# Kernel optimization log

Hardware: AMD Instinct MI355X
Metric: run time of the kernel (lower is better)

Reference implementation:

```python
import jax, jax.numpy as jnp
import numpy as np

H = 512                      # hidden_dim
C, T, F = 2, 128, 257        # output_dims
FLAT = C * T * F             # 65792 flattened spectrogram frame
CD, SD = 256, 256            # content_dim, style_dim
D_IN = CD + SD + FLAT        # GRU input size


def setup_inputs() -> dict:
    key = jax.random.key(0)
    ks = jax.random.split(key, 8)
    B, S = 4, 16
    sc = 0.02  # small init so tanh/sigmoid stay in a sane range
    return {
        "content_emb": jax.random.normal(ks[0], (B, S, CD), jnp.float32),
        "style_emb": jax.random.normal(ks[1], (B, SD), jnp.float32),
        "start_token": jax.random.normal(ks[2], (FLAT,), jnp.float32),
        "W_ih": jax.random.normal(ks[3], (3 * H, D_IN), jnp.float32) * sc,
        "W_hh": jax.random.normal(ks[4], (3 * H, H), jnp.float32) * sc,
        "b_ih": jnp.zeros((3 * H,), jnp.float32),
        "b_hh": jnp.zeros((3 * H,), jnp.float32),
        "W_proj": jax.random.normal(ks[5], (FLAT, H), jnp.float32) * sc,
        "b_proj": jnp.zeros((FLAT,), jnp.float32),
    }


def _gru_cell(x, h, W_ih, W_hh, b_ih, b_hh):
    # PyTorch GRU gate order: r, z, n
    gi = x @ W_ih.T + b_ih          # (B, 3H)
    gh = h @ W_hh.T + b_hh          # (B, 3H)
    i_r, i_z, i_n = jnp.split(gi, 3, axis=-1)
    h_r, h_z, h_n = jnp.split(gh, 3, axis=-1)
    r = jax.nn.sigmoid(i_r + h_r)
    z = jax.nn.sigmoid(i_z + h_z)
    n = jnp.tanh(i_n + r * h_n)
    return (1.0 - z) * n + z * h


def reference(content_emb, style_emb, start_token, W_ih, W_hh, b_ih, b_hh, W_proj, b_proj):
    B, S, _ = content_emb.shape
    h0 = jnp.zeros((B, H), content_emb.dtype)
    prev0 = jnp.broadcast_to(start_token, (B, FLAT))

    def step(carry, c_s):
        h, prev = carry
        # concat [content_s, style, prev_output] -> (B, D_IN)
        x = jnp.concatenate([c_s, style_emb, prev], axis=-1)
        h = _gru_cell(x, h, W_ih, W_hh, b_ih, b_hh)
        out = h @ W_proj.T + b_proj   # (B, FLAT)
        return (h, out), out

    _, outs = jax.lax.scan(step, (h0, prev0), jnp.swapaxes(content_emb, 0, 1))
    outs = jnp.swapaxes(outs, 0, 1)   # (B, S, FLAT)
    return outs.reshape(B, S, C, T, F)
```

## Files before the change

kernel.cpp:

```cpp
#include <hip/hip_runtime.h>
#include <hip/hip_bf16.h>
#include <math.h>

typedef __bf16 bf16x8 __attribute__((ext_vector_type(8)));
typedef float  f32x4  __attribute__((ext_vector_type(4)));

#define HDIM   512
#define FLAT   65792
#define DIN    66304
#define G3     1536
#define NSLAB  2056
#define NPAD   544
#define LPITCH 40
#define MT     128
#define KSPLIT 21
#define CHUNK  98

#define BH_BYTES  71581696ULL
#define MBUF_BYTES 3342336ULL
#define GIB_BYTES   393216ULL
#define HALL_BYTES  131072ULL
#define HBF_BYTES    65536ULL

__device__ __forceinline__ ushort f2bf(float f) {
    uint u = __float_as_uint(f);
    u += 0x7FFFu + ((u >> 16) & 1u);
    return (ushort)(u >> 16);
}

__global__ __launch_bounds__(256) void buildBh(const float* __restrict__ Wp,
                                               const float* __restrict__ bproj,
                                               const float* __restrict__ start,
                                               ushort* __restrict__ Bh) {
    __shared__ ushort tr[512 * 33];
    const int slab = blockIdx.x;
    const int tid  = threadIdx.x;
    for (int idx = tid; idx < 32 * 512; idx += 256) {
        const int k = idx >> 9;
        const int n = idx & 511;
        tr[n * 33 + k] = f2bf(Wp[(size_t)(slab * 32 + k) * 512 + n]);
    }
    __syncthreads();
    uint* out = (uint*)(Bh + (size_t)slab * 17408);
    for (int d = tid; d < 8704; d += 256) {
        const int n  = d >> 4;
        const int k2 = (d & 15) * 2;
        ushort lo, hi;
        if (n < 512)      { lo = tr[n * 33 + k2];            hi = tr[n * 33 + k2 + 1]; }
        else if (n == 512){ lo = f2bf(bproj[slab * 32 + k2]); hi = f2bf(bproj[slab * 32 + k2 + 1]); }
        else if (n == 513){ lo = f2bf(start[slab * 32 + k2]); hi = f2bf(start[slab * 32 + k2 + 1]); }
        else              { lo = 0; hi = 0; }
        out[d] = (uint)lo | ((uint)hi << 16);
    }
}

__global__ __launch_bounds__(1024) void gemmM(const float* __restrict__ Wih,
                                              const ushort* __restrict__ Bh,
                                              float* __restrict__ Mbuf) {
    __shared__ ushort Alds[MT * LPITCH];
    __shared__ ushort Blds[NPAD * LPITCH];
    const int tid  = threadIdx.x;
    const int lane = tid & 63;
    const int wave = tid >> 6;
    const int wm   = wave >> 1;
    const int wn   = wave & 1;
    const int lrow = lane & 15;
    const int quad = lane >> 4;
    const int bid   = blockIdx.x;
    const int mtile = bid % 12;
    const int kc    = bid / 12;
    const int s0 = kc * CHUNK;
    const int s1 = min(s0 + CHUNK, NSLAB);

    const int arow = tid >> 3;
    const int aseg = tid & 7;
    const float* aPtr = Wih + (size_t)(mtile * MT + arow) * DIN + 512 + aseg * 4;

    f32x4 acc[17];
#pragma unroll
    for (int t = 0; t < 17; ++t) acc[t] = (f32x4){0.f, 0.f, 0.f, 0.f};

    float4 aReg;
    uint4  bReg0 = {}, bReg1 = {}, bReg2 = {};
    {
        const size_t sb = (size_t)s0 * 17408;
        aReg  = *(const float4*)(aPtr + (size_t)s0 * 32);
        bReg0 = *(const uint4*)(Bh + sb + (size_t)tid * 8);
        bReg1 = *(const uint4*)(Bh + sb + (size_t)(tid + 1024) * 8);
        if (tid < 128) bReg2 = *(const uint4*)(Bh + sb + (size_t)(tid + 2048) * 8);
    }
    for (int s = s0; s < s1; ++s) {
        {
            uint2 ap;
            ap.x = (uint)f2bf(aReg.x) | ((uint)f2bf(aReg.y) << 16);
            ap.y = (uint)f2bf(aReg.z) | ((uint)f2bf(aReg.w) << 16);
            *(uint2*)&Alds[arow * LPITCH + aseg * 4] = ap;
            *(uint4*)&Blds[(tid >> 2) * LPITCH + (tid & 3) * 8] = bReg0;
            const int c1 = tid + 1024;
            *(uint4*)&Blds[(c1 >> 2) * LPITCH + (c1 & 3) * 8] = bReg1;
            if (tid < 128) {
                const int c2 = tid + 2048;
                *(uint4*)&Blds[(c2 >> 2) * LPITCH + (c2 & 3) * 8] = bReg2;
            }
        }
        __syncthreads();
        if (s + 1 < s1) {
            const size_t sb = (size_t)(s + 1) * 17408;
            aReg  = *(const float4*)(aPtr + (size_t)(s + 1) * 32);
            bReg0 = *(const uint4*)(Bh + sb + (size_t)tid * 8);
            bReg1 = *(const uint4*)(Bh + sb + (size_t)(tid + 1024) * 8);
            if (tid < 128) bReg2 = *(const uint4*)(Bh + sb + (size_t)(tid + 2048) * 8);
        }
        const bf16x8 af = __builtin_bit_cast(bf16x8,
            *(const uint4*)&Alds[(wm * 16 + lrow) * LPITCH + quad * 8]);
#pragma unroll
        for (int t = 0; t < 17; ++t) {
            const bf16x8 bf = __builtin_bit_cast(bf16x8,
                *(const uint4*)&Blds[(wn * 272 + t * 16 + lrow) * LPITCH + quad * 8]);
            acc[t] = __builtin_amdgcn_mfma_f32_16x16x32_bf16(af, bf, acc[t], 0, 0, 0);
        }
        __syncthreads();
    }
#pragma unroll
    for (int t = 0; t < 17; ++t) {
        const int col = wn * 272 + t * 16 + lrow;
#pragma unroll
        for (int r = 0; r < 4; ++r) {
            const int row = mtile * MT + wm * 16 + quad * 4 + r;
            atomicAdd(&Mbuf[(size_t)row * NPAD + col], acc[t][r]);
        }
    }
}

__global__ __launch_bounds__(1024) void gemmMDirect(const float* __restrict__ Wih,
                                                    const float* __restrict__ Wp,
                                                    const float* __restrict__ bproj,
                                                    const float* __restrict__ start,
                                                    float* __restrict__ Mbuf) {
    __shared__ ushort Alds[MT * LPITCH];
    __shared__ ushort Blds[NPAD * LPITCH];
    const int tid  = threadIdx.x;
    const int lane = tid & 63;
    const int wave = tid >> 6;
    const int wm   = wave >> 1;
    const int wn   = wave & 1;
    const int lrow = lane & 15;
    const int quad = lane >> 4;
    const int bid   = blockIdx.x;
    const int mtile = bid % 12;
    const int kc    = bid / 12;
    const int s0 = kc * CHUNK;
    const int s1 = min(s0 + CHUNK, NSLAB);

    const int arow = tid >> 3;
    const int aseg = tid & 7;
    const float* aPtr = Wih + (size_t)(mtile * MT + arow) * DIN + 512 + aseg * 4;

    const int bk = tid >> 5;
    const int bn0 = (tid & 31) * 4;
    const int ek = tid & 31;
    const float* esrc = (tid < 32) ? bproj : start;

    for (int idx = tid; idx < 30 * LPITCH; idx += 1024) Blds[514 * LPITCH + idx] = 0;

    f32x4 acc[17];
#pragma unroll
    for (int t = 0; t < 17; ++t) acc[t] = (f32x4){0.f, 0.f, 0.f, 0.f};

    float4 aReg;
    float4 bReg[4];
    float  eReg = 0.f;
    {
        aReg = *(const float4*)(aPtr + (size_t)s0 * 32);
        const float* bbase = Wp + (size_t)(s0 * 32 + bk) * 512 + bn0;
#pragma unroll
        for (int q = 0; q < 4; ++q) bReg[q] = *(const float4*)(bbase + q * 128);
        if (tid < 64) eReg = esrc[s0 * 32 + ek];
    }
    for (int s = s0; s < s1; ++s) {
        {
            uint2 ap;
            ap.x = (uint)f2bf(aReg.x) | ((uint)f2bf(aReg.y) << 16);
            ap.y = (uint)f2bf(aReg.z) | ((uint)f2bf(aReg.w) << 16);
            *(uint2*)&Alds[arow * LPITCH + aseg * 4] = ap;
#pragma unroll
            for (int q = 0; q < 4; ++q) {
                const int n = bn0 + q * 128;
                Blds[(n + 0) * LPITCH + bk] = f2bf(bReg[q].x);
                Blds[(n + 1) * LPITCH + bk] = f2bf(bReg[q].y);
                Blds[(n + 2) * LPITCH + bk] = f2bf(bReg[q].z);
                Blds[(n + 3) * LPITCH + bk] = f2bf(bReg[q].w);
            }
            if (tid < 64) Blds[(512 + (tid >> 5)) * LPITCH + ek] = f2bf(eReg);
        }
        __syncthreads();
        if (s + 1 < s1) {
            aReg = *(const float4*)(aPtr + (size_t)(s + 1) * 32);
            const float* bbase = Wp + (size_t)((s + 1) * 32 + bk) * 512 + bn0;
#pragma unroll
            for (int q = 0; q < 4; ++q) bReg[q] = *(const float4*)(bbase + q * 128);
            if (tid < 64) eReg = esrc[(s + 1) * 32 + ek];
        }
        const bf16x8 af = __builtin_bit_cast(bf16x8,
            *(const uint4*)&Alds[(wm * 16 + lrow) * LPITCH + quad * 8]);
#pragma unroll
        for (int t = 0; t < 17; ++t) {
            const bf16x8 bf = __builtin_bit_cast(bf16x8,
                *(const uint4*)&Blds[(wn * 272 + t * 16 + lrow) * LPITCH + quad * 8]);
            acc[t] = __builtin_amdgcn_mfma_f32_16x16x32_bf16(af, bf, acc[t], 0, 0, 0);
        }
        __syncthreads();
    }
#pragma unroll
    for (int t = 0; t < 17; ++t) {
        const int col = wn * 272 + t * 16 + lrow;
#pragma unroll
        for (int r = 0; r < 4; ++r) {
            const int row = mtile * MT + wm * 16 + quad * 4 + r;
            atomicAdd(&Mbuf[(size_t)row * NPAD + col], acc[t][r]);
        }
    }
}

__global__ __launch_bounds__(256) void giBase(const float* __restrict__ Wih,
                                              const float* __restrict__ content,
                                              const float* __restrict__ style,
                                              const float* __restrict__ bih,
                                              const float* __restrict__ Mbuf,
                                              float* __restrict__ giB) {
    const int j = (blockIdx.x * blockDim.x + threadIdx.x) >> 6;
    if (j >= G3) return;
    const int lane = threadIdx.x & 63;
    const int b = lane >> 4;
    const int s = lane & 15;
    const float* wr = Wih + (size_t)j * DIN;
    const float* cp = content + (size_t)lane * 256;
    const float* sp = style + (size_t)b * 256;
    float acc = 0.f;
#pragma unroll 4
    for (int d = 0; d < 256; d += 4) {
        const float4 w = *(const float4*)(wr + d);
        const float4 x = *(const float4*)(cp + d);
        acc += w.x * x.x + w.y * x.y + w.z * x.z + w.w * x.w;
    }
#pragma unroll 4
    for (int d = 0; d < 256; d += 4) {
        const float4 w = *(const float4*)(wr + 256 + d);
        const float4 x = *(const float4*)(sp + d);
        acc += w.x * x.x + w.y * x.y + w.z * x.z + w.w * x.w;
    }
    acc += bih[j] + ((s == 0) ? Mbuf[(size_t)j * NPAD + 513] : Mbuf[(size_t)j * NPAD + 512]);
    giB[(size_t)lane * G3 + j] = acc;
}

__global__ __launch_bounds__(256) void stepK(const float* __restrict__ Mbuf,
                                             const float* __restrict__ Whh,
                                             const float* __restrict__ bhh,
                                             const float* __restrict__ giB,
                                             float* __restrict__ hAll,
                                             ushort* __restrict__ hBf,
                                             const int s) {
    const int gw   = (blockIdx.x * blockDim.x + threadIdx.x) >> 6;
    const int lane = threadIdx.x & 63;
    const int b = gw & 3;
    const int j = gw >> 2;
    float dMr = 0.f, dMz = 0.f, dMn = 0.f, dWr = 0.f, dWz = 0.f, dWn = 0.f;
    if (s > 0) {
        const float* h = hAll + (size_t)((s - 1) * 4 + b) * HDIM;
        float hr[8];
#pragma unroll
        for (int i = 0; i < 8; ++i) hr[i] = h[i * 64 + lane];
        const float* M0 = Mbuf + (size_t)j * NPAD;
        const float* M1 = Mbuf + (size_t)(j + 512) * NPAD;
        const float* M2 = Mbuf + (size_t)(j + 1024) * NPAD;
        const float* W0 = Whh + (size_t)j * HDIM;
        const float* W1 = Whh + (size_t)(j + 512) * HDIM;
        const float* W2 = Whh + (size_t)(j + 1024) * HDIM;
#pragma unroll
        for (int i = 0; i < 8; ++i) {
            const int d = i * 64 + lane;
            dMr += M0[d] * hr[i]; dMz += M1[d] * hr[i]; dMn += M2[d] * hr[i];
            dWr += W0[d] * hr[i]; dWz += W1[d] * hr[i]; dWn += W2[d] * hr[i];
        }
#pragma unroll
        for (int m = 1; m < 64; m <<= 1) {
            dMr += __shfl_xor(dMr, m); dMz += __shfl_xor(dMz, m); dMn += __shfl_xor(dMn, m);
            dWr += __shfl_xor(dWr, m); dWz += __shfl_xor(dWz, m); dWn += __shfl_xor(dWn, m);
        }
    }
    if (lane == 0) {
        const float* gb = giB + (size_t)(b * 16 + s) * G3;
        const float gir = gb[j] + dMr;
        const float giz = gb[j + 512] + dMz;
        const float gin = gb[j + 1024] + dMn;
        const float ghr = bhh[j] + dWr;
        const float ghz = bhh[j + 512] + dWz;
        const float ghn = bhh[j + 1024] + dWn;
        const float r = 1.f / (1.f + expf(-(gir + ghr)));
        const float z = 1.f / (1.f + expf(-(giz + ghz)));
        const float n = tanhf(gin + r * ghn);
        const float hp = (s > 0) ? hAll[(size_t)((s - 1) * 4 + b) * HDIM + j] : 0.f;
        const float hn = (1.f - z) * n + z * hp;
        hAll[(size_t)(s * 4 + b) * HDIM + j] = hn;
        hBf[(size_t)(s * 4 + b) * HDIM + j] = f2bf(hn);
    }
}

__global__ __launch_bounds__(256) void projK(const float* __restrict__ Wp,
                                             const float* __restrict__ bproj,
                                             const ushort* __restrict__ hBf,
                                             float* __restrict__ out) {
    const int lane = threadIdx.x & 63;
    const int wave = threadIdx.x >> 6;
    const int f0   = blockIdx.x * 256 + wave * 64;
    const int lrow = lane & 15;
    const int quad = lane >> 4;
    f32x4 acc[4][4];
#pragma unroll
    for (int pt = 0; pt < 4; ++pt)
#pragma unroll
        for (int ft = 0; ft < 4; ++ft) acc[pt][ft] = (f32x4){0.f, 0.f, 0.f, 0.f};

    for (int d0 = 0; d0 < HDIM; d0 += 32) {
        bf16x8 afr[4];
#pragma unroll
        for (int pt = 0; pt < 4; ++pt)
            afr[pt] = __builtin_bit_cast(bf16x8,
                *(const uint4*)(hBf + (size_t)(pt * 16 + lrow) * HDIM + d0 + quad * 8));
#pragma unroll
        for (int ft = 0; ft < 4; ++ft) {
            const float* wrow = Wp + (size_t)(f0 + ft * 16 + lrow) * HDIM + d0 + quad * 8;
            const float4 w0 = *(const float4*)(wrow);
            const float4 w1 = *(const float4*)(wrow + 4);
            uint4 pr;
            pr.x = (uint)f2bf(w0.x) | ((uint)f2bf(w0.y) << 16);
            pr.y = (uint)f2bf(w0.z) | ((uint)f2bf(w0.w) << 16);
            pr.z = (uint)f2bf(w1.x) | ((uint)f2bf(w1.y) << 16);
            pr.w = (uint)f2bf(w1.z) | ((uint)f2bf(w1.w) << 16);
            const bf16x8 bfr = __builtin_bit_cast(bf16x8, pr);
#pragma unroll
            for (int pt = 0; pt < 4; ++pt)
                acc[pt][ft] = __builtin_amdgcn_mfma_f32_16x16x32_bf16(afr[pt], bfr, acc[pt][ft], 0, 0, 0);
        }
    }
#pragma unroll
    for (int pt = 0; pt < 4; ++pt)
#pragma unroll
        for (int ft = 0; ft < 4; ++ft) {
            const int f = f0 + ft * 16 + lrow;
            const float bp = bproj[f];
#pragma unroll
            for (int r = 0; r < 4; ++r) {
                const int p = pt * 16 + quad * 4 + r;
                const int ss = p >> 2;
                const int bb = p & 3;
                out[(size_t)(bb * 16 + ss) * FLAT + f] = acc[pt][ft][r] + bp;
            }
        }
}

extern "C" void kernel_launch(void* const* d_in, const int* in_sizes, int n_in,
                              void* d_out, int out_size, void* d_ws, size_t ws_size,
                              hipStream_t stream) {
    const float* content = (const float*)d_in[0];
    const float* style   = (const float*)d_in[1];
    const float* start   = (const float*)d_in[2];
    const float* Wih     = (const float*)d_in[3];
    const float* Whh     = (const float*)d_in[4];
    const float* bih     = (const float*)d_in[5];
    const float* bhh     = (const float*)d_in[6];
    const float* Wproj   = (const float*)d_in[7];
    const float* bproj   = (const float*)d_in[8];
    float* out = (float*)d_out;

    const size_t needFast = BH_BYTES + MBUF_BYTES + GIB_BYTES + HALL_BYTES + HBF_BYTES;
    const bool fast = (ws_size >= needFast);

    char* ws = (char*)d_ws;
    const size_t base = fast ? BH_BYTES : 0;
    ushort* Bh   = (ushort*)ws;
    float*  Mbuf = (float*)(ws + base);
    float*  giB  = (float*)(ws + base + MBUF_BYTES);
    float*  hAll = (float*)(ws + base + MBUF_BYTES + GIB_BYTES);
    ushort* hBf  = (ushort*)(ws + base + MBUF_BYTES + GIB_BYTES + HALL_BYTES);

    hipMemsetAsync(Mbuf, 0, MBUF_BYTES, stream);
    if (fast) {
        buildBh<<<NSLAB, 256, 0, stream>>>(Wproj, bproj, start, Bh);
        gemmM<<<12 * KSPLIT, 1024, 0, stream>>>(Wih, Bh, Mbuf);
    } else {
        gemmMDirect<<<12 * KSPLIT, 1024, 0, stream>>>(Wih, Wproj, bproj, start, Mbuf);
    }
    giBase<<<384, 256, 0, stream>>>(Wih, content, style, bih, Mbuf, giB);
    for (int s = 0; s < 16; ++s)
        stepK<<<512, 256, 0, stream>>>(Mbuf, Whh, bhh, giB, hAll, hBf, s);
    projK<<<FLAT / 256, 256, 0, stream>>>(Wproj, bproj, hBf, out);
}
```

Measured before the change: 933.5 us.

## Fuse 16 GRU recurrence step launches into one cooperative kernel with grid sync

Replaces the 16 per-timestep stepK launches with a single cooperative kernel that loops over timesteps and separates them with grid.sync. Each wave loads its Mbuf and W_hh rows into registers once, instead of re-reading them from memory every step. This removes per-step launch overhead and the repeated weight traffic, at the cost of a grid-wide barrier per step and a dependence on cooperative launch support. If the cooperative launch fails, the code falls back to the original loop of 16 launches.

```diff
diff --git a/kernel.cpp b/kernel.cpp
--- a/kernel.cpp
+++ b/kernel.cpp
@@ -1,6 +1,9 @@
 #include <hip/hip_runtime.h>
 #include <hip/hip_bf16.h>
+#include <hip/hip_cooperative_groups.h>
 #include <math.h>
+
+namespace cg = cooperative_groups;
 
 typedef __bf16 bf16x8 __attribute__((ext_vector_type(8)));
 typedef float  f32x4  __attribute__((ext_vector_type(4)));
@@ -253,6 +256,69 @@
     giB[(size_t)lane * G3 + j] = acc;
 }
 
+__global__ __launch_bounds__(256) void stepsFused(const float* __restrict__ Mbuf,
+                                                  const float* __restrict__ Whh,
+                                                  const float* __restrict__ bhh,
+                                                  const float* __restrict__ giB,
+                                                  float* __restrict__ hAll,
+                                                  ushort* __restrict__ hBf) {
+    cg::grid_group grid = cg::this_grid();
+    const int gw   = (blockIdx.x * blockDim.x + threadIdx.x) >> 6;
+    const int lane = threadIdx.x & 63;
+    const int b = gw & 3;
+    const int j = gw >> 2;
+
+    const float* M0 = Mbuf + (size_t)j * NPAD;
+    const float* M1 = Mbuf + (size_t)(j + 512) * NPAD;
+    const float* M2 = Mbuf + (size_t)(j + 1024) * NPAD;
+    const float* W0 = Whh + (size_t)j * HDIM;
+    const float* W1 = Whh + (size_t)(j + 512) * HDIM;
+    const float* W2 = Whh + (size_t)(j + 1024) * HDIM;
+    float m0[8], m1[8], m2[8], w0[8], w1[8], w2[8];
+#pragma unroll
+    for (int i = 0; i < 8; ++i) {
+        const int d = i * 64 + lane;
+        m0[i] = M0[d]; m1[i] = M1[d]; m2[i] = M2[d];
+        w0[i] = W0[d]; w1[i] = W1[d]; w2[i] = W2[d];
+    }
+    const float bh0 = bhh[j], bh1 = bhh[j + 512], bh2 = bhh[j + 1024];
+
+    for (int s = 0; s < 16; ++s) {
+        float dMr = 0.f, dMz = 0.f, dMn = 0.f, dWr = 0.f, dWz = 0.f, dWn = 0.f;
+        if (s > 0) {
+            const float* h = hAll + (size_t)((s - 1) * 4 + b) * HDIM;
+            float hr[8];
+#pragma unroll
+            for (int i = 0; i < 8; ++i) hr[i] = h[i * 64 + lane];
+#pragma unroll
+            for (int i = 0; i < 8; ++i) {
+                dMr += m0[i] * hr[i]; dMz += m1[i] * hr[i]; dMn += m2[i] * hr[i];
+                dWr += w0[i] * hr[i]; dWz += w1[i] * hr[i]; dWn += w2[i] * hr[i];
+            }
+#pragma unroll
+            for (int m = 1; m < 64; m <<= 1) {
+                dMr += __shfl_xor(dMr, m); dMz += __shfl_xor(dMz, m); dMn += __shfl_xor(dMn, m);
+                dWr += __shfl_xor(dWr, m); dWz += __shfl_xor(dWz, m); dWn += __shfl_xor(dWn, m);
+            }
+        }
+        if (lane == 0) {
+            const float* gb = giB + (size_t)(b * 16 + s) * G3;
+            const float gir = gb[j] + dMr;
+            const float giz = gb[j + 512] + dMz;
+            const float gin = gb[j + 1024] + dMn;
+            const float r = 1.f / (1.f + expf(-(gir + bh0 + dWr)));
+            const float z = 1.f / (1.f + expf(-(giz + bh1 + dWz)));
+            const float n = tanhf(gin + r * (bh2 + dWn));
+            const float hp = (s > 0) ? hAll[(size_t)((s - 1) * 4 + b) * HDIM + j] : 0.f;
+            const float hn = (1.f - z) * n + z * hp;
+            hAll[(size_t)(s * 4 + b) * HDIM + j] = hn;
+            hBf[(size_t)(s * 4 + b) * HDIM + j] = f2bf(hn);
+        }
+        __threadfence();
+        grid.sync();
+    }
+}
+
 __global__ __launch_bounds__(256) void stepK(const float* __restrict__ Mbuf,
                                              const float* __restrict__ Whh,
                                              const float* __restrict__ bhh,
@@ -392,7 +458,18 @@
         gemmMDirect<<<12 * KSPLIT, 1024, 0, stream>>>(Wih, Wproj, bproj, start, Mbuf);
     }
     giBase<<<384, 256, 0, stream>>>(Wih, content, style, bih, Mbuf, giB);
-    for (int s = 0; s < 16; ++s)
-        stepK<<<512, 256, 0, stream>>>(Mbuf, Whh, bhh, giB, hAll, hBf, s);
+
+    {
+        const float* MbufC = Mbuf;
+        const float* giBC  = giB;
+        void* args[] = { (void*)&MbufC, (void*)&Whh, (void*)&bhh,
+                         (void*)&giBC, (void*)&hAll, (void*)&hBf };
+        hipError_t e = hipLaunchCooperativeKernel((const void*)stepsFused,
+                                                  dim3(512), dim3(256), args, 0, stream);
+        if (e != hipSuccess) {
+            for (int s = 0; s < 16; ++s)
+                stepK<<<512, 256, 0, stream>>>(Mbuf, Whh, bhh, giB, hAll, hBf, s);
+        }
+    }
     projK<<<FLAT / 256, 256, 0, stream>>>(Wproj, bproj, hBf, out);
 }
```

Measured after the change: 2.320 ms. 149% more time.

## Retile GEMM waves to 32x144 tiles for A/B fragment reuse

Applied to the files above, without the earlier changes.

Changes the per-wave tile in the precompute GEMMs from 16x272 to 32x144, so each B fragment read from LDS feeds two MFMAs and each wave reads less B per slab. This requires padding N from 544 to 576, which grows the precomputed bf16 Bh buffer and Mbuf and adds extra zero columns of work. It targets LDS read bandwidth in the MFMA inner loop, in exchange for more padded MFMA work, more HBM traffic for Bh and more atomics.

```diff
diff --git a/kernel.cpp b/kernel.cpp
--- a/kernel.cpp
+++ b/kernel.cpp
@@ -10,14 +10,15 @@
 #define DIN    66304
 #define G3     1536
 #define NSLAB  2056
-#define NPAD   544
+#define NPAD   576
 #define LPITCH 40
 #define MT     128
 #define KSPLIT 21
 #define CHUNK  98
-
-#define BH_BYTES  71581696ULL
-#define MBUF_BYTES 3342336ULL
+#define SLABU  18432
+
+#define BH_BYTES  75792384ULL
+#define MBUF_BYTES 3538944ULL
 #define GIB_BYTES   393216ULL
 #define HALL_BYTES  131072ULL
 #define HBF_BYTES    65536ULL
@@ -41,8 +42,8 @@
         tr[n * 33 + k] = f2bf(Wp[(size_t)(slab * 32 + k) * 512 + n]);
     }
     __syncthreads();
-    uint* out = (uint*)(Bh + (size_t)slab * 17408);
-    for (int d = tid; d < 8704; d += 256) {
+    uint* out = (uint*)(Bh + (size_t)slab * SLABU);
+    for (int d = tid; d < (SLABU / 2); d += 256) {
         const int n  = d >> 4;
         const int k2 = (d & 15) * 2;
         ushort lo, hi;
@@ -62,8 +63,8 @@
     const int tid  = threadIdx.x;
     const int lane = tid & 63;
     const int wave = tid >> 6;
-    const int wm   = wave >> 1;
-    const int wn   = wave & 1;
+    const int wm2  = wave >> 2;
+    const int wn2  = wave & 3;
     const int lrow = lane & 15;
     const int quad = lane >> 4;
     const int bid   = blockIdx.x;
@@ -76,18 +77,20 @@
     const int aseg = tid & 7;
     const float* aPtr = Wih + (size_t)(mtile * MT + arow) * DIN + 512 + aseg * 4;
 
-    f32x4 acc[17];
-#pragma unroll
-    for (int t = 0; t < 17; ++t) acc[t] = (f32x4){0.f, 0.f, 0.f, 0.f};
+    f32x4 acc[2][9];
+#pragma unroll
+    for (int p = 0; p < 2; ++p)
+#pragma unroll
+        for (int t = 0; t < 9; ++t) acc[p][t] = (f32x4){0.f, 0.f, 0.f, 0.f};
 
     float4 aReg;
     uint4  bReg0 = {}, bReg1 = {}, bReg2 = {};
     {
-        const size_t sb = (size_t)s0 * 17408;
+        const size_t sb = (size_t)s0 * SLABU;
         aReg  = *(const float4*)(aPtr + (size_t)s0 * 32);
         bReg0 = *(const uint4*)(Bh + sb + (size_t)tid * 8);
         bReg1 = *(const uint4*)(Bh + sb + (size_t)(tid + 1024) * 8);
-        if (tid < 128) bReg2 = *(const uint4*)(Bh + sb + (size_t)(tid + 2048) * 8);
+        if (tid < 256) bReg2 = *(const uint4*)(Bh + sb + (size_t)(tid + 2048) * 8);
     }
     for (int s = s0; s < s1; ++s) {
         {
@@ -98,38 +101,44 @@
             *(uint4*)&Blds[(tid >> 2) * LPITCH + (tid & 3) * 8] = bReg0;
             const int c1 = tid + 1024;
             *(uint4*)&Blds[(c1 >> 2) * LPITCH + (c1 & 3) * 8] = bReg1;
-            if (tid < 128) {
+            if (tid < 256) {
                 const int c2 = tid + 2048;
                 *(uint4*)&Blds[(c2 >> 2) * LPITCH + (c2 & 3) * 8] = bReg2;
             }
         }
         __syncthreads();
         if (s + 1 < s1) {
-            const size_t sb = (size_t)(s + 1) * 17408;
+            const size_t sb = (size_t)(s + 1) * SLABU;
             aReg  = *(const float4*)(aPtr + (size_t)(s + 1) * 32);
             bReg0 = *(const uint4*)(Bh + sb + (size_t)tid * 8);
             bReg1 = *(const uint4*)(Bh + sb + (size_t)(tid + 1024) * 8);
-            if (tid < 128) bReg2 = *(const uint4*)(Bh + sb + (size_t)(tid + 2048) * 8);
-        }
-        const bf16x8 af = __builtin_bit_cast(bf16x8,
-            *(const uint4*)&Alds[(wm * 16 + lrow) * LPITCH + quad * 8]);
-#pragma unroll
-        for (int t = 0; t < 17; ++t) {
+            if (tid < 256) bReg2 = *(const uint4*)(Bh + sb + (size_t)(tid + 2048) * 8);
+        }
+        bf16x8 af[2];
+#pragma unroll
+        for (int p = 0; p < 2; ++p)
+            af[p] = __builtin_bit_cast(bf16x8,
+                *(const uint4*)&Alds[(wm2 * 32 + p * 16 + lrow) * LPITCH + quad * 8]);
+#pragma unroll
+        for (int t = 0; t < 9; ++t) {
             const bf16x8 bf = __builtin_bit_cast(bf16x8,
-                *(const uint4*)&Blds[(wn * 272 + t * 16 + lrow) * LPITCH + quad * 8]);
-            acc[t] = __builtin_amdgcn_mfma_f32_16x16x32_bf16(af, bf, acc[t], 0, 0, 0);
+                *(const uint4*)&Blds[(wn2 * 144 + t * 16 + lrow) * LPITCH + quad * 8]);
+            acc[0][t] = __builtin_amdgcn_mfma_f32_16x16x32_bf16(af[0], bf, acc[0][t], 0, 0, 0);
+            acc[1][t] = __builtin_amdgcn_mfma_f32_16x16x32_bf16(af[1], bf, acc[1][t], 0, 0, 0);
         }
         __syncthreads();
     }
 #pragma unroll
-    for (int t = 0; t < 17; ++t) {
-        const int col = wn * 272 + t * 16 + lrow;
-#pragma unroll
-        for (int r = 0; r < 4; ++r) {
-            const int row = mtile * MT + wm * 16 + quad * 4 + r;
-            atomicAdd(&Mbuf[(size_t)row * NPAD + col], acc[t][r]);
-        }
-    }
+    for (int p = 0; p < 2; ++p)
+#pragma unroll
+        for (int t = 0; t < 9; ++t) {
+            const int col = wn2 * 144 + t * 16 + lrow;
+#pragma unroll
+            for (int r = 0; r < 4; ++r) {
+                const int row = mtile * MT + wm2 * 32 + p * 16 + quad * 4 + r;
+                atomicAdd(&Mbuf[(size_t)row * NPAD + col], acc[p][t][r]);
+            }
+        }
 }
 
 __global__ __launch_bounds__(1024) void gemmMDirect(const float* __restrict__ Wih,
@@ -142,8 +151,8 @@
     const int tid  = threadIdx.x;
     const int lane = tid & 63;
     const int wave = tid >> 6;
-    const int wm   = wave >> 1;
-    const int wn   = wave & 1;
+    const int wm2  = wave >> 2;
+    const int wn2  = wave & 3;
     const int lrow = lane & 15;
     const int quad = lane >> 4;
     const int bid   = blockIdx.x;
@@ -156,16 +165,18 @@
     const int aseg = tid & 7;
     const float* aPtr = Wih + (size_t)(mtile * MT + arow) * DIN + 512 + aseg * 4;
 
-    const int bk = tid >> 5;
+    const int bk  = tid >> 5;
     const int bn0 = (tid & 31) * 4;
-    const int ek = tid & 31;
+    const int ek  = tid & 31;
     const float* esrc = (tid < 32) ? bproj : start;
 
-    for (int idx = tid; idx < 30 * LPITCH; idx += 1024) Blds[514 * LPITCH + idx] = 0;
-
-    f32x4 acc[17];
-#pragma unroll
-    for (int t = 0; t < 17; ++t) acc[t] = (f32x4){0.f, 0.f, 0.f, 0.f};
+    for (int idx = tid; idx < 62 * LPITCH; idx += 1024) Blds[514 * LPITCH + idx] = 0;
+
+    f32x4 acc[2][9];
+#pragma unroll
+    for (int p = 0; p < 2; ++p)
+#pragma unroll
+        for (int t = 0; t < 9; ++t) acc[p][t] = (f32x4){0.f, 0.f, 0.f, 0.f};
 
     float4 aReg;
     float4 bReg[4];
@@ -201,25 +212,31 @@
             for (int q = 0; q < 4; ++q) bReg[q] = *(const float4*)(bbase + q * 128);
             if (tid < 64) eReg = esrc[(s + 1) * 32 + ek];
         }
-        const bf16x8 af = __builtin_bit_cast(bf16x8,
-            *(const uint4*)&Alds[(wm * 16 + lrow) * LPITCH + quad * 8]);
-#pragma unroll
-        for (int t = 0; t < 17; ++t) {
+        bf16x8 af[2];
+#pragma unroll
+        for (int p = 0; p < 2; ++p)
+            af[p] = __builtin_bit_cast(bf16x8,
+                *(const uint4*)&Alds[(wm2 * 32 + p * 16 + lrow) * LPITCH + quad * 8]);
+#pragma unroll
+        for (int t = 0; t < 9; ++t) {
             const bf16x8 bf = __builtin_bit_cast(bf16x8,
-                *(const uint4*)&Blds[(wn * 272 + t * 16 + lrow) * LPITCH + quad * 8]);
-            acc[t] = __builtin_amdgcn_mfma_f32_16x16x32_bf16(af, bf, acc[t], 0, 0, 0);
+                *(const uint4*)&Blds[(wn2 * 144 + t * 16 + lrow) * LPITCH + quad * 8]);
+            acc[0][t] = __builtin_amdgcn_mfma_f32_16x16x32_bf16(af[0], bf, acc[0][t], 0, 0, 0);
+            acc[1][t] = __builtin_amdgcn_mfma_f32_16x16x32_bf16(af[1], bf, acc[1][t], 0, 0, 0);
         }
         __syncthreads();
     }
 #pragma unroll
-    for (int t = 0; t < 17; ++t) {
-        const int col = wn * 272 + t * 16 + lrow;
-#pragma unroll
-        for (int r = 0; r < 4; ++r) {
-            const int row = mtile * MT + wm * 16 + quad * 4 + r;
-            atomicAdd(&Mbuf[(size_t)row * NPAD + col], acc[t][r]);
-        }
-    }
+    for (int p = 0; p < 2; ++p)
+#pragma unroll
+        for (int t = 0; t < 9; ++t) {
+            const int col = wn2 * 144 + t * 16 + lrow;
+#pragma unroll
+            for (int r = 0; r < 4; ++r) {
+                const int row = mtile * MT + wm2 * 32 + p * 16 + quad * 4 + r;
+                atomicAdd(&Mbuf[(size_t)row * NPAD + col], acc[p][t][r]);
+            }
+        }
 }
 
 __global__ __launch_bounds__(256) void giBase(const float* __restrict__ Wih,
```

After: 921.6 us. Within noise of the previous version (-1.3%).
